# Kernel tuning notes

Measured on AMD Instinct MI355X. Metric: run time of the kernel, lower is better.

The kernel has to match this reference:

```python
import jax, jax.numpy as jnp
import numpy as np

GROUP = 32  # hadamard_group_size == MXFP4 block size
FP4_GRID = np.array([0.0, 0.5, 1.0, 1.5, 2.0, 3.0, 4.0, 6.0], dtype=np.float32)  # e2m1 magnitudes
FP4_MID = np.array([0.25, 0.75, 1.25, 1.75, 2.5, 3.5, 5.0], dtype=np.float32)    # RTN midpoints


def _hadamard(n):
    # Sylvester construction, normalized so H is orthonormal (matches hadamard(n)*n**-0.5)
    H = np.array([[1.0]], dtype=np.float64)
    while H.shape[0] < n:
        H = np.block([[H, H], [H, -H]])
    return (H / np.sqrt(n)).astype(np.float32)


def _pseudo_quant_mxfp4(t, H, gs):
    """Hadamard-rotate per group of 32, then MXFP4 (e2m1 + power-of-two block scale)
    quant-dequant with abs_max scaling and a global scale. STE through the rounding."""
    shp = t.shape
    rot = t.reshape(-1, GROUP) @ H                      # [n_groups, 32] rotated space
    v = jax.lax.stop_gradient(rot) * gs
    absmax = jnp.max(jnp.abs(v), axis=-1, keepdims=True)
    # E8M0 power-of-two shared scale so that absmax/scale <= 6 (max e2m1 value)
    scale = jnp.exp2(jnp.ceil(jnp.log2(absmax / 6.0 + 1e-30)))
    scale = jnp.where(absmax > 0, scale, 1.0)
    u = v / scale
    grid = jnp.asarray(FP4_GRID)
    mid = jnp.asarray(FP4_MID)
    q = jnp.sign(u) * grid[jnp.searchsorted(mid, jnp.abs(u))]  # round-to-nearest e2m1
    dq = q * scale / gs
    out = rot + jax.lax.stop_gradient(dq - rot)         # straight-through estimator
    return out.reshape(shp)


def setup_inputs() -> dict:
    key = jax.random.key(0)
    kx, kw, kb = jax.random.split(key, 3)
    B, S, K, N = 4, 2048, 4096, 4096
    x = jax.random.normal(kx, (B, S, K), jnp.float32)
    weight = jax.random.normal(kw, (N, K), jnp.float32) * (K ** -0.5)
    bias = jax.random.normal(kb, (N,), jnp.float32)
    H = jnp.asarray(_hadamard(GROUP))
    weight_global_scale = jnp.array([3.0], jnp.float32)  # abs_max method
    act_global_scale = jnp.array([3.0], jnp.float32)
    return {"x": x, "weight": weight, "bias": bias, "hadamard_matrix": H,
            "weight_global_scale": weight_global_scale, "act_global_scale": act_global_scale}


def reference(x, weight, bias, hadamard_matrix, weight_global_scale, act_global_scale):
    x_dq = _pseudo_quant_mxfp4(x, hadamard_matrix, act_global_scale[0])
    w_dq = _pseudo_quant_mxfp4(weight, hadamard_matrix, weight_global_scale[0])
    # both operands stay in the rotated space; per-group Hadamard is orthogonal so
    # x_rot @ w_rot^T == x @ w^T up to quantization error (QuTLASS semantics)
    return jnp.einsum('bsk,nk->bsn', x_dq, w_dq) + bias
```

## Files before the change

### kernel.cpp

```cpp
#include <hip/hip_runtime.h>
#include <hip/hip_bf16.h>

typedef int   i32x4  __attribute__((ext_vector_type(4)));
typedef int   i32x8  __attribute__((ext_vector_type(8)));
typedef float f32x16 __attribute__((ext_vector_type(16)));

__device__ inline void gload_lds16(const void* g, void* l) {
  __builtin_amdgcn_global_load_lds((const __attribute__((address_space(1))) void*)g,
                                   (__attribute__((address_space(3))) void*)l, 16, 0, 0);
}
__device__ inline void gload_lds4(const void* g, void* l) {
  __builtin_amdgcn_global_load_lds((const __attribute__((address_space(1))) void*)g,
                                   (__attribute__((address_space(3))) void*)l, 4, 0, 0);
}
__device__ inline i32x8 pad8(i32x4 v) {
  i32x8 r;
  r[0] = v[0]; r[1] = v[1]; r[2] = v[2]; r[3] = v[3];
  r[4] = 0; r[5] = 0; r[6] = 0; r[7] = 0;
  return r;
}

__global__ __launch_bounds__(256) void quant_pack_fp4(const float* __restrict__ in,
                                                      unsigned char* __restrict__ outq,
                                                      unsigned char* __restrict__ outsc,
                                                      const float* __restrict__ gs_ptr,
                                                      int n_groups, int rows, int kg) {
  int g = blockIdx.x * 256 + threadIdx.x;
  const float gs = gs_ptr[0];
  int r = g / kg, j = g - r * kg;

  float t[32];
  const float4* p4 = (const float4*)(in + (size_t)g * 32);
#pragma unroll
  for (int i = 0; i < 8; ++i) {
    float4 v4 = p4[i];
    t[4 * i + 0] = v4.x; t[4 * i + 1] = v4.y;
    t[4 * i + 2] = v4.z; t[4 * i + 3] = v4.w;
  }
#pragma unroll
  for (int s = 0; s < 5; ++s) {
    const int hh = 1 << s;
#pragma unroll
    for (int i = 0; i < 32; ++i) {
      if ((i & hh) == 0) {
        float a = t[i], b = t[i + hh];
        t[i] = a + b;
        t[i + hh] = a - b;
      }
    }
  }

  const float c = 0.17677669529663687f;
  float v[32];
  float am = 0.0f;
#pragma unroll
  for (int i = 0; i < 32; ++i) {
    float vi = (t[i] * c) * gs;
    v[i] = vi;
    am = fmaxf(am, fabsf(vi));
  }

  float a6 = am / 6.0f;
  int ex;
  float mant = frexpf(a6, &ex);
  int e = (mant == 0.5f) ? ex - 1 : ex;
  if (e < -127) e = -127;
  if (e > 127) e = 127;
  float inv_s = ldexpf(1.0f, -e);

  unsigned int dw[4] = {0u, 0u, 0u, 0u};
#pragma unroll
  for (int i = 0; i < 32; ++i) {
    float u = v[i] * inv_s;
    float au = fabsf(u);
    int idx = (au > 0.25f) + (au > 0.75f) + (au > 1.25f) + (au > 1.75f)
            + (au > 2.5f) + (au > 3.5f) + (au > 5.0f);
    int code = idx | ((u < 0.0f) ? 8 : 0);
    dw[i >> 3] |= (unsigned)code << ((i & 7) * 4);
  }
  i32x4 packed;
  packed[0] = (int)dw[0]; packed[1] = (int)dw[1];
  packed[2] = (int)dw[2]; packed[3] = (int)dw[3];
  *(i32x4*)(outq + (size_t)r * ((size_t)kg * 16) + (size_t)j * 16) = packed;

  int s = j >> 3, j0 = j & 7;
  int p = ((j0 & 1) << 2) | (j0 >> 1);
  if (kg == 128) {
    __shared__ unsigned char sl[256];
    sl[(s << 4) | ((r & 1) << 3) | p] = (unsigned char)(e + 127);
    __syncthreads();
    if (threadIdx.x < 64) {
      int si = threadIdx.x >> 2, wd = threadIdx.x & 3;
      unsigned int vv = *(const unsigned int*)&sl[(si << 4) | (wd << 2)];
      size_t r0 = (size_t)blockIdx.x * 2;
      *(unsigned int*)(outsc + ((size_t)si * rows + r0) * 8 + (wd << 2)) = vv;
    }
  } else {
    outsc[((size_t)s * rows + r) * 8 + p] = (unsigned char)(e + 127);
  }
}


#define STAGE(mb, kt, h, ldsHalf) do {                                               \
    const unsigned char* _s = (mb) + (size_t)((h)*64 + (w << 3) + (l >> 3)) * KB2    \
                      + (size_t)(kt) * 128 + (size_t)csw * 16;                       \
    gload_lds16(_s, (unsigned char*)(ldsHalf) + (w << 10));                          \
    gload_lds16(_s + ((size_t)KB2 << 5), (unsigned char*)(ldsHalf) + (w << 10) + 4096); \
  } while (0)

#define STAGE_ASC(kt, bf) gload_lds4(AscG + ((size_t)(kt) * M + brow) * 8 + (tid << 2), \
                                     (unsigned char*)&asc[bf][0] + (w << 8))
#define STAGE_BSC(kt, bf) gload_lds4(BscG + ((size_t)(kt) * N + bcol) * 8 + (tid << 2), \
                                     (unsigned char*)&bsc[bf][0] + (w << 8))

#define LOADB(bf) do {                                                               \
    const unsigned char* _bb = &lds[bf][1][0][0];                                    \
    _Pragma("unroll")                                                                \
    for (int nt = 0; nt < 2; ++nt) {                                                 \
      int row = wn * 64 + nt * 32 + (l & 31);                                        \
      int xr = row & 7;                                                              \
      _Pragma("unroll")                                                              \
      for (int kk = 0; kk < 4; ++kk)                                                 \
        bfr[nt][kk] = *(const i32x4*)(_bb + row * 128 + (((kk * 2 + h) ^ xr) << 4)); \
      sb[nt] = *(const int*)((const unsigned char*)&bsc[bf][0] + row * 8 + h * 4);   \
    } } while (0)

#define LOADA(bf, mt) do {                                                           \
    const unsigned char* _ab = &lds[bf][0][0][0];                                    \
    int row = wm * 64 + (mt) * 32 + (l & 31);                                        \
    int xr = row & 7;                                                                \
    _Pragma("unroll")                                                                \
    for (int kk = 0; kk < 4; ++kk)                                                   \
      af[kk] = *(const i32x4*)(_ab + row * 128 + (((kk * 2 + h) ^ xr) << 4));        \
    sa = *(const int*)((const unsigned char*)&asc[bf][0] + row * 8 + h * 4);         \
  } while (0)

#define MF1(mt, nt, kk)                                                              \
  acc[mt][nt] = __builtin_amdgcn_mfma_scale_f32_32x32x64_f8f6f4(                     \
      pad8(af[kk]), pad8(bfr[nt][kk]), acc[mt][nt], 4, 4, kk, sa, kk, sb[nt]);

#define MFMAQ(mt) do {                                                               \
    __builtin_amdgcn_s_setprio(1);                                                   \
    MF1(mt, 0, 0) MF1(mt, 1, 0) MF1(mt, 0, 1) MF1(mt, 1, 1)                          \
    MF1(mt, 0, 2) MF1(mt, 1, 2) MF1(mt, 0, 3) MF1(mt, 1, 3)                          \
    __builtin_amdgcn_s_setprio(0);                                                   \
  } while (0)

#define MIDSYNC() do { __builtin_amdgcn_s_barrier();                                 \
    asm volatile("s_waitcnt lgkmcnt(0)" ::: "memory");                               \
    __builtin_amdgcn_sched_barrier(0); } while (0)

#define ENDP() __builtin_amdgcn_s_barrier()
#define VM10() asm volatile("s_waitcnt vmcnt(10)" ::: "memory")

__global__ __launch_bounds__(256, 2) void gemm128_fp4(const unsigned char* __restrict__ Aq,
                                                      const unsigned char* __restrict__ Bq,
                                                      const unsigned char* __restrict__ AscG,
                                                      const unsigned char* __restrict__ BscG,
                                                      float* __restrict__ C,
                                                      const float* __restrict__ bias,
                                                      const float* __restrict__ gsx,
                                                      const float* __restrict__ gsw,
                                                      int M, int N, int K) {
  __shared__ __align__(16) unsigned char lds[2][2][2][8192];
  __shared__ __align__(16) unsigned char asc[2][1024];
  __shared__ __align__(16) unsigned char bsc[2][1024];

  const int tid = threadIdx.x;
  const int w = tid >> 6, l = tid & 63;
  const int wm = w >> 1, wn = w & 1;
  const int h = l >> 5;
  const int csw = (l & 7) ^ (l >> 3);
  const int KB2 = K >> 1;

  const int ntn = N >> 7;
  const int nwg = gridDim.x;
  int r_t, c_t;
  {
    int bid = blockIdx.x;
    if ((nwg & 7) == 0) {
      int x = bid & 7, o = bid >> 3, cpx = nwg >> 3;
      int rpx = cpx / ntn;
      if ((ntn & 7) == 0 && rpx > 0 && (cpx % ntn) == 0) {
        int g8 = o & 7, rr = (o >> 3) % rpx, ss = o / (8 * rpx);
        r_t = x * rpx + rr;
        c_t = ss * 8 + g8;
      } else {
        int lin = x * cpx + o;
        r_t = lin / ntn; c_t = lin % ntn;
      }
    } else {
      r_t = bid / ntn; c_t = bid % ntn;
    }
  }
  const size_t brow = (size_t)r_t * 128;
  const size_t bcol = (size_t)c_t * 128;

  const unsigned char* Ab = Aq + brow * (size_t)KB2;
  const unsigned char* Bb = Bq + bcol * (size_t)KB2;

  f32x16 acc[2][2];
#pragma unroll
  for (int m = 0; m < 2; ++m)
#pragma unroll
    for (int n = 0; n < 2; ++n)
#pragma unroll
      for (int r = 0; r < 16; ++r) acc[m][n][r] = 0.0f;

  i32x4 af[4], bfr[2][4];
  int sa, sb[2];

  const int nkt = K / 256;

  STAGE(Ab, 0, 0, &lds[0][0][0][0]); STAGE(Ab, 0, 1, &lds[0][0][1][0]); STAGE_ASC(0, 0);
  STAGE(Bb, 0, 0, &lds[0][1][0][0]); STAGE(Bb, 0, 1, &lds[0][1][1][0]); STAGE_BSC(0, 0);
  STAGE(Bb, 1, 0, &lds[1][1][0][0]); STAGE(Bb, 1, 1, &lds[1][1][1][0]); STAGE_BSC(1, 1);
  STAGE(Ab, 1, 0, &lds[1][0][0][0]); STAGE(Ab, 1, 1, &lds[1][0][1][0]); STAGE_ASC(1, 1);
  VM10();
  __builtin_amdgcn_s_barrier();

  for (int t = 0; t < nkt; ++t) {
    const int p = t & 1;
    const int t2 = (t + 2 < nkt) ? t + 2 : nkt - 1;

    LOADB(p); LOADA(p, 0);
    MIDSYNC();
    STAGE(Bb, t2, 0, &lds[p][1][0][0]);
    STAGE(Bb, t2, 1, &lds[p][1][1][0]);
    STAGE_BSC(t2, p);
    MFMAQ(0);
    ENDP();

    LOADA(p, 1);
    MIDSYNC();
    STAGE(Ab, t2, 0, &lds[p][0][0][0]);
    STAGE(Ab, t2, 1, &lds[p][0][1][0]);
    STAGE_ASC(t2, p);
    MFMAQ(1);
    VM10();
    ENDP();
  }

  const float inv = 1.0f / (gsx[0] * gsw[0]);
#pragma unroll
  for (int nt = 0; nt < 2; ++nt) {
    const int col = (int)bcol + wn * 64 + nt * 32 + (l & 31);
    const float bv = bias[col];
#pragma unroll
    for (int mt = 0; mt < 2; ++mt) {
      const size_t rbase = brow + (size_t)(wm * 64 + mt * 32 + 4 * h);
#pragma unroll
      for (int r = 0; r < 16; ++r) {
        const size_t row = rbase + (r & 3) + 8 * (r >> 2);
        C[row * (size_t)N + col] = acc[mt][nt][r] * inv + bv;
      }
    }
  }
}

extern "C" void kernel_launch(void* const* d_in, const int* in_sizes, int n_in,
                              void* d_out, int out_size, void* d_ws, size_t ws_size,
                              hipStream_t stream) {
  const float* x    = (const float*)d_in[0];
  const float* wgt  = (const float*)d_in[1];
  const float* bias = (const float*)d_in[2];
  const float* wgs  = (const float*)d_in[4];
  const float* ags  = (const float*)d_in[5];

  const int N = in_sizes[2];
  const int K = in_sizes[1] / N;
  const int M = in_sizes[0] / K;
  const int kg = K / 32;

  unsigned char* aq  = (unsigned char*)d_ws;
  unsigned char* bq  = aq + (size_t)M * (K / 2);
  unsigned char* asc = bq + (size_t)N * (K / 2);
  unsigned char* bsc = asc + (size_t)M * kg;

  const int xg = in_sizes[0] / 32;
  const int wg = in_sizes[1] / 32;
  quant_pack_fp4<<<dim3((xg + 255) / 256), dim3(256), 0, stream>>>(x, aq, asc, ags, xg, M, kg);
  quant_pack_fp4<<<dim3((wg + 255) / 256), dim3(256), 0, stream>>>(wgt, bq, bsc, wgs, wg, N, kg);

  dim3 grid((M / 128) * (N / 128));
  gemm128_fp4<<<grid, dim3(256), 0, stream>>>(aq, bq, asc, bsc, (float*)d_out, bias,
                                              ags, wgs, M, N, K);
}
```

Measured before the change: 155.9 us.

## Double-buffer MFMA fragments in registers and fuse the two quant kernels

The GEMM main loop now processes two K-tiles per iteration. It keeps two register sets of A/B fragments and scales, so LDS reads for the next tile are issued while MFMAs run on the current one. Each stage loads a full A+B tile set at once, with adjusted vmcnt/lgkmcnt waits and fewer barriers per tile. Separately, the activation and weight quantization kernels are merged into a single launch that picks its input by block index. This removes one launch and lets the two quantizations overlap. The cost is more register pressure from the doubled fragment storage, which may affect occupancy at two blocks per CU.

```diff
diff --git a/kernel.cpp b/kernel.cpp
--- a/kernel.cpp
+++ b/kernel.cpp
@@ -20,14 +20,25 @@
   return r;
 }
 
-__global__ __launch_bounds__(256) void quant_pack_fp4(const float* __restrict__ in,
-                                                      unsigned char* __restrict__ outq,
-                                                      unsigned char* __restrict__ outsc,
-                                                      const float* __restrict__ gs_ptr,
-                                                      int n_groups, int rows, int kg) {
-  int g = blockIdx.x * 256 + threadIdx.x;
-  const float gs = gs_ptr[0];
-  int r = g / kg, j = g - r * kg;
+__global__ __launch_bounds__(256) void quant_fused(const float* __restrict__ x,
+                                                   const float* __restrict__ wt,
+                                                   unsigned char* __restrict__ xq,
+                                                   unsigned char* __restrict__ xsc,
+                                                   unsigned char* __restrict__ wq,
+                                                   unsigned char* __restrict__ wsc,
+                                                   const float* __restrict__ ags,
+                                                   const float* __restrict__ wgs,
+                                                   int xg, int Mrows, int Nrows, int kg) {
+  const int first = blockIdx.x * 256;
+  const bool isX = first < xg;
+  const float* in        = isX ? x   : wt;
+  unsigned char* outq    = isX ? xq  : wq;
+  unsigned char* outsc   = isX ? xsc : wsc;
+  const float gs         = isX ? ags[0] : wgs[0];
+  const int rows         = isX ? Mrows : Nrows;
+  const int base         = isX ? first : first - xg;
+  const int g = base + threadIdx.x;
+  const int r = g / kg, j = g - r * kg;
 
   float t[32];
   const float4* p4 = (const float4*)(in + (size_t)g * 32);
@@ -92,7 +103,7 @@
     if (threadIdx.x < 64) {
       int si = threadIdx.x >> 2, wd = threadIdx.x & 3;
       unsigned int vv = *(const unsigned int*)&sl[(si << 4) | (wd << 2)];
-      size_t r0 = (size_t)blockIdx.x * 2;
+      size_t r0 = (size_t)(base / 128);
       *(unsigned int*)(outsc + ((size_t)si * rows + r0) * 8 + (wd << 2)) = vv;
     }
   } else {
@@ -113,7 +124,14 @@
 #define STAGE_BSC(kt, bf) gload_lds4(BscG + ((size_t)(kt) * N + bcol) * 8 + (tid << 2), \
                                      (unsigned char*)&bsc[bf][0] + (w << 8))
 
-#define LOADB(bf) do {                                                               \
+#define STAGESET(kt, bf) do {                                                        \
+    STAGE(Ab, kt, 0, &lds[bf][0][0][0]); STAGE(Ab, kt, 1, &lds[bf][0][1][0]);        \
+    STAGE_ASC(kt, bf);                                                               \
+    STAGE(Bb, kt, 0, &lds[bf][1][0][0]); STAGE(Bb, kt, 1, &lds[bf][1][1][0]);        \
+    STAGE_BSC(kt, bf);                                                               \
+  } while (0)
+
+#define READFRAGS(bf, AF, BF, SA, SB) do {                                           \
     const unsigned char* _bb = &lds[bf][1][0][0];                                    \
     _Pragma("unroll")                                                                \
     for (int nt = 0; nt < 2; ++nt) {                                                 \
@@ -121,37 +139,41 @@
       int xr = row & 7;                                                              \
       _Pragma("unroll")                                                              \
       for (int kk = 0; kk < 4; ++kk)                                                 \
-        bfr[nt][kk] = *(const i32x4*)(_bb + row * 128 + (((kk * 2 + h) ^ xr) << 4)); \
-      sb[nt] = *(const int*)((const unsigned char*)&bsc[bf][0] + row * 8 + h * 4);   \
-    } } while (0)
-
-#define LOADA(bf, mt) do {                                                           \
+        BF[nt][kk] = *(const i32x4*)(_bb + row * 128 + (((kk * 2 + h) ^ xr) << 4));  \
+      SB[nt] = *(const int*)((const unsigned char*)&bsc[bf][0] + row * 8 + h * 4);   \
+    }                                                                                \
     const unsigned char* _ab = &lds[bf][0][0][0];                                    \
-    int row = wm * 64 + (mt) * 32 + (l & 31);                                        \
-    int xr = row & 7;                                                                \
     _Pragma("unroll")                                                                \
-    for (int kk = 0; kk < 4; ++kk)                                                   \
-      af[kk] = *(const i32x4*)(_ab + row * 128 + (((kk * 2 + h) ^ xr) << 4));        \
-    sa = *(const int*)((const unsigned char*)&asc[bf][0] + row * 8 + h * 4);         \
+    for (int mt = 0; mt < 2; ++mt) {                                                 \
+      int row = wm * 64 + mt * 32 + (l & 31);                                        \
+      int xr = row & 7;                                                              \
+      _Pragma("unroll")                                                              \
+      for (int kk = 0; kk < 4; ++kk)                                                 \
+        AF[mt][kk] = *(const i32x4*)(_ab + row * 128 + (((kk * 2 + h) ^ xr) << 4));  \
+      SA[mt] = *(const int*)((const unsigned char*)&asc[bf][0] + row * 8 + h * 4);   \
+    }                                                                                \
   } while (0)
 
-#define MF1(mt, nt, kk)                                                              \
+#define MF1(AF, BF, SA, SB, mt, nt, kk)                                              \
   acc[mt][nt] = __builtin_amdgcn_mfma_scale_f32_32x32x64_f8f6f4(                     \
-      pad8(af[kk]), pad8(bfr[nt][kk]), acc[mt][nt], 4, 4, kk, sa, kk, sb[nt]);
-
-#define MFMAQ(mt) do {                                                               \
+      pad8(AF[mt][kk]), pad8(BF[nt][kk]), acc[mt][nt], 4, 4, kk, SA[mt], kk, SB[nt]);
+
+#define MFMAQ_ALL(AF, BF, SA, SB) do {                                               \
     __builtin_amdgcn_s_setprio(1);                                                   \
-    MF1(mt, 0, 0) MF1(mt, 1, 0) MF1(mt, 0, 1) MF1(mt, 1, 1)                          \
-    MF1(mt, 0, 2) MF1(mt, 1, 2) MF1(mt, 0, 3) MF1(mt, 1, 3)                          \
+    MF1(AF, BF, SA, SB, 0, 0, 0) MF1(AF, BF, SA, SB, 0, 1, 0)                        \
+    MF1(AF, BF, SA, SB, 1, 0, 0) MF1(AF, BF, SA, SB, 1, 1, 0)                        \
+    MF1(AF, BF, SA, SB, 0, 0, 1) MF1(AF, BF, SA, SB, 0, 1, 1)                        \
+    MF1(AF, BF, SA, SB, 1, 0, 1) MF1(AF, BF, SA, SB, 1, 1, 1)                        \
+    MF1(AF, BF, SA, SB, 0, 0, 2) MF1(AF, BF, SA, SB, 0, 1, 2)                        \
+    MF1(AF, BF, SA, SB, 1, 0, 2) MF1(AF, BF, SA, SB, 1, 1, 2)                        \
+    MF1(AF, BF, SA, SB, 0, 0, 3) MF1(AF, BF, SA, SB, 0, 1, 3)                        \
+    MF1(AF, BF, SA, SB, 1, 0, 3) MF1(AF, BF, SA, SB, 1, 1, 3)                        \
     __builtin_amdgcn_s_setprio(0);                                                   \
   } while (0)
 
-#define MIDSYNC() do { __builtin_amdgcn_s_barrier();                                 \
-    asm volatile("s_waitcnt lgkmcnt(0)" ::: "memory");                               \
+#define LGKM0() do { asm volatile("s_waitcnt lgkmcnt(0)" ::: "memory");              \
     __builtin_amdgcn_sched_barrier(0); } while (0)
-
-#define ENDP() __builtin_amdgcn_s_barrier()
-#define VM10() asm volatile("s_waitcnt vmcnt(10)" ::: "memory")
+#define VM6()  asm volatile("s_waitcnt vmcnt(6)" ::: "memory")
 
 __global__ __launch_bounds__(256, 2) void gemm128_fp4(const unsigned char* __restrict__ Aq,
                                                       const unsigned char* __restrict__ Bq,
@@ -207,38 +229,38 @@
 #pragma unroll
       for (int r = 0; r < 16; ++r) acc[m][n][r] = 0.0f;
 
-  i32x4 af[4], bfr[2][4];
-  int sa, sb[2];
+  i32x4 afA[2][4], bfrA[2][4];  int saA[2], sbA[2];
+  i32x4 afB[2][4], bfrB[2][4];  int saB[2], sbB[2];
 
   const int nkt = K / 256;
 
-  STAGE(Ab, 0, 0, &lds[0][0][0][0]); STAGE(Ab, 0, 1, &lds[0][0][1][0]); STAGE_ASC(0, 0);
-  STAGE(Bb, 0, 0, &lds[0][1][0][0]); STAGE(Bb, 0, 1, &lds[0][1][1][0]); STAGE_BSC(0, 0);
-  STAGE(Bb, 1, 0, &lds[1][1][0][0]); STAGE(Bb, 1, 1, &lds[1][1][1][0]); STAGE_BSC(1, 1);
-  STAGE(Ab, 1, 0, &lds[1][0][0][0]); STAGE(Ab, 1, 1, &lds[1][0][1][0]); STAGE_ASC(1, 1);
-  VM10();
+  STAGESET(0, 0);
+  STAGESET(1, 1);
+  VM6();
   __builtin_amdgcn_s_barrier();
-
-  for (int t = 0; t < nkt; ++t) {
-    const int p = t & 1;
+  READFRAGS(0, afA, bfrA, saA, sbA);
+  LGKM0();
+  __builtin_amdgcn_s_barrier();
+
+  for (int t = 0; t < nkt; t += 2) {
     const int t2 = (t + 2 < nkt) ? t + 2 : nkt - 1;
-
-    LOADB(p); LOADA(p, 0);
-    MIDSYNC();
-    STAGE(Bb, t2, 0, &lds[p][1][0][0]);
-    STAGE(Bb, t2, 1, &lds[p][1][1][0]);
-    STAGE_BSC(t2, p);
-    MFMAQ(0);
-    ENDP();
-
-    LOADA(p, 1);
-    MIDSYNC();
-    STAGE(Ab, t2, 0, &lds[p][0][0][0]);
-    STAGE(Ab, t2, 1, &lds[p][0][1][0]);
-    STAGE_ASC(t2, p);
-    MFMAQ(1);
-    VM10();
-    ENDP();
+    const int t3 = (t + 3 < nkt) ? t + 3 : nkt - 1;
+
+    STAGESET(t2, 0);
+    VM6();
+    __builtin_amdgcn_s_barrier();
+    READFRAGS(1, afB, bfrB, saB, sbB);
+    MFMAQ_ALL(afA, bfrA, saA, sbA);
+    LGKM0();
+    __builtin_amdgcn_s_barrier();
+
+    STAGESET(t3, 1);
+    VM6();
+    __builtin_amdgcn_s_barrier();
+    READFRAGS(0, afA, bfrA, saA, sbA);
+    MFMAQ_ALL(afB, bfrB, saB, sbB);
+    LGKM0();
+    __builtin_amdgcn_s_barrier();
   }
 
   const float inv = 1.0f / (gsx[0] * gsw[0]);
@@ -279,8 +301,8 @@
 
   const int xg = in_sizes[0] / 32;
   const int wg = in_sizes[1] / 32;
-  quant_pack_fp4<<<dim3((xg + 255) / 256), dim3(256), 0, stream>>>(x, aq, asc, ags, xg, M, kg);
-  quant_pack_fp4<<<dim3((wg + 255) / 256), dim3(256), 0, stream>>>(wgt, bq, bsc, wgs, wg, N, kg);
+  quant_fused<<<dim3((xg + wg) / 256), dim3(256), 0, stream>>>(
+      x, wgt, aq, asc, bq, bsc, ags, wgs, xg, M, N, kg);
 
   dim3 grid((M / 128) * (N / 128));
   gemm128_fp4<<<grid, dim3(256), 0, stream>>>(aq, bq, asc, bsc, (float*)d_out, bias,
```

New measurement: 166.0 us. 6.5% more time.

## Load B operand directly from global to registers and fuse quant launches

Applied to the files above, without the earlier changes.

The GEMM no longer stages the B tile and its scales through LDS. Each wave reads its B fragments and scales straight from global memory into two register sets, which double-buffer B across k-tiles. The main loop is unrolled by two and the vmcnt wait threshold is raised to match the extra loads. The two quantization launches are merged into one grid that splits blocks between x and the weight, removing a kernel launch. In exchange, B is read uncoalesced from global memory and replicated across waves, and register pressure rises.

```diff
diff --git a/kernel.cpp b/kernel.cpp
--- a/kernel.cpp
+++ b/kernel.cpp
@@ -20,14 +20,25 @@
   return r;
 }
 
-__global__ __launch_bounds__(256) void quant_pack_fp4(const float* __restrict__ in,
-                                                      unsigned char* __restrict__ outq,
-                                                      unsigned char* __restrict__ outsc,
-                                                      const float* __restrict__ gs_ptr,
-                                                      int n_groups, int rows, int kg) {
-  int g = blockIdx.x * 256 + threadIdx.x;
-  const float gs = gs_ptr[0];
-  int r = g / kg, j = g - r * kg;
+__global__ __launch_bounds__(256) void quant_fused(const float* __restrict__ x,
+                                                   const float* __restrict__ wt,
+                                                   unsigned char* __restrict__ xq,
+                                                   unsigned char* __restrict__ xsc,
+                                                   unsigned char* __restrict__ wq,
+                                                   unsigned char* __restrict__ wsc,
+                                                   const float* __restrict__ ags,
+                                                   const float* __restrict__ wgs,
+                                                   int xg, int Mrows, int Nrows, int kg) {
+  const int first = blockIdx.x * 256;
+  const bool isX = first < xg;
+  const float* in        = isX ? x   : wt;
+  unsigned char* outq    = isX ? xq  : wq;
+  unsigned char* outsc   = isX ? xsc : wsc;
+  const float gs         = isX ? ags[0] : wgs[0];
+  const int rows         = isX ? Mrows : Nrows;
+  const int base         = isX ? first : first - xg;
+  const int g = base + threadIdx.x;
+  const int r = g / kg, j = g - r * kg;
 
   float t[32];
   const float4* p4 = (const float4*)(in + (size_t)g * 32);
@@ -92,7 +103,7 @@
     if (threadIdx.x < 64) {
       int si = threadIdx.x >> 2, wd = threadIdx.x & 3;
       unsigned int vv = *(const unsigned int*)&sl[(si << 4) | (wd << 2)];
-      size_t r0 = (size_t)blockIdx.x * 2;
+      size_t r0 = (size_t)(base / 128);
       *(unsigned int*)(outsc + ((size_t)si * rows + r0) * 8 + (wd << 2)) = vv;
     }
   } else {
@@ -101,8 +112,8 @@
 }
 
 
-#define STAGE(mb, kt, h, ldsHalf) do {                                               \
-    const unsigned char* _s = (mb) + (size_t)((h)*64 + (w << 3) + (l >> 3)) * KB2    \
+#define STAGE_A(kt, h, ldsHalf) do {                                                 \
+    const unsigned char* _s = Ab + (size_t)((h)*64 + (w << 3) + (l >> 3)) * KB2      \
                       + (size_t)(kt) * 128 + (size_t)csw * 16;                       \
     gload_lds16(_s, (unsigned char*)(ldsHalf) + (w << 10));                          \
     gload_lds16(_s + ((size_t)KB2 << 5), (unsigned char*)(ldsHalf) + (w << 10) + 4096); \
@@ -110,23 +121,25 @@
 
 #define STAGE_ASC(kt, bf) gload_lds4(AscG + ((size_t)(kt) * M + brow) * 8 + (tid << 2), \
                                      (unsigned char*)&asc[bf][0] + (w << 8))
-#define STAGE_BSC(kt, bf) gload_lds4(BscG + ((size_t)(kt) * N + bcol) * 8 + (tid << 2), \
-                                     (unsigned char*)&bsc[bf][0] + (w << 8))
-
-#define LOADB(bf) do {                                                               \
-    const unsigned char* _bb = &lds[bf][1][0][0];                                    \
+
+#define STAGESET_A(kt, bf) do {                                                      \
+    STAGE_A(kt, 0, &lds[bf][0][0]); STAGE_A(kt, 1, &lds[bf][1][0]);                  \
+    STAGE_ASC(kt, bf);                                                               \
+  } while (0)
+
+#define LOADBF(kt, BF, SB) do {                                                      \
     _Pragma("unroll")                                                                \
     for (int nt = 0; nt < 2; ++nt) {                                                 \
       int row = wn * 64 + nt * 32 + (l & 31);                                        \
-      int xr = row & 7;                                                              \
+      const unsigned char* _bp = Bb + (size_t)row * KB2 + (size_t)(kt) * 128 + (h << 4); \
       _Pragma("unroll")                                                              \
       for (int kk = 0; kk < 4; ++kk)                                                 \
-        bfr[nt][kk] = *(const i32x4*)(_bb + row * 128 + (((kk * 2 + h) ^ xr) << 4)); \
-      sb[nt] = *(const int*)((const unsigned char*)&bsc[bf][0] + row * 8 + h * 4);   \
+        BF[nt][kk] = *(const i32x4*)(_bp + (kk << 5));                               \
+      SB[nt] = *(const int*)(BscG + ((size_t)(kt) * N + bcol + row) * 8 + (h << 2)); \
     } } while (0)
 
 #define LOADA(bf, mt) do {                                                           \
-    const unsigned char* _ab = &lds[bf][0][0][0];                                    \
+    const unsigned char* _ab = &lds[bf][0][0];                                       \
     int row = wm * 64 + (mt) * 32 + (l & 31);                                        \
     int xr = row & 7;                                                                \
     _Pragma("unroll")                                                                \
@@ -135,14 +148,16 @@
     sa = *(const int*)((const unsigned char*)&asc[bf][0] + row * 8 + h * 4);         \
   } while (0)
 
-#define MF1(mt, nt, kk)                                                              \
+#define MF1(mt, nt, kk, BF, SB)                                                      \
   acc[mt][nt] = __builtin_amdgcn_mfma_scale_f32_32x32x64_f8f6f4(                     \
-      pad8(af[kk]), pad8(bfr[nt][kk]), acc[mt][nt], 4, 4, kk, sa, kk, sb[nt]);
-
-#define MFMAQ(mt) do {                                                               \
+      pad8(af[kk]), pad8(BF[nt][kk]), acc[mt][nt], 4, 4, kk, sa, kk, SB[nt]);
+
+#define MFMAQ(mt, BF, SB) do {                                                       \
     __builtin_amdgcn_s_setprio(1);                                                   \
-    MF1(mt, 0, 0) MF1(mt, 1, 0) MF1(mt, 0, 1) MF1(mt, 1, 1)                          \
-    MF1(mt, 0, 2) MF1(mt, 1, 2) MF1(mt, 0, 3) MF1(mt, 1, 3)                          \
+    MF1(mt, 0, 0, BF, SB) MF1(mt, 1, 0, BF, SB)                                      \
+    MF1(mt, 0, 1, BF, SB) MF1(mt, 1, 1, BF, SB)                                      \
+    MF1(mt, 0, 2, BF, SB) MF1(mt, 1, 2, BF, SB)                                      \
+    MF1(mt, 0, 3, BF, SB) MF1(mt, 1, 3, BF, SB)                                      \
     __builtin_amdgcn_s_setprio(0);                                                   \
   } while (0)
 
@@ -151,7 +166,7 @@
     __builtin_amdgcn_sched_barrier(0); } while (0)
 
 #define ENDP() __builtin_amdgcn_s_barrier()
-#define VM10() asm volatile("s_waitcnt vmcnt(10)" ::: "memory")
+#define VM13() asm volatile("s_waitcnt vmcnt(13)" ::: "memory")
 
 __global__ __launch_bounds__(256, 2) void gemm128_fp4(const unsigned char* __restrict__ Aq,
                                                       const unsigned char* __restrict__ Bq,
@@ -162,9 +177,8 @@
                                                       const float* __restrict__ gsx,
                                                       const float* __restrict__ gsw,
                                                       int M, int N, int K) {
-  __shared__ __align__(16) unsigned char lds[2][2][2][8192];
+  __shared__ __align__(16) unsigned char lds[2][2][8192];
   __shared__ __align__(16) unsigned char asc[2][1024];
-  __shared__ __align__(16) unsigned char bsc[2][1024];
 
   const int tid = threadIdx.x;
   const int w = tid >> 6, l = tid & 63;
@@ -207,37 +221,41 @@
 #pragma unroll
       for (int r = 0; r < 16; ++r) acc[m][n][r] = 0.0f;
 
-  i32x4 af[4], bfr[2][4];
-  int sa, sb[2];
+  i32x4 af[4];
+  int sa;
+  i32x4 bfX[2][4], bfY[2][4];
+  int sbX[2], sbY[2];
 
   const int nkt = K / 256;
 
-  STAGE(Ab, 0, 0, &lds[0][0][0][0]); STAGE(Ab, 0, 1, &lds[0][0][1][0]); STAGE_ASC(0, 0);
-  STAGE(Bb, 0, 0, &lds[0][1][0][0]); STAGE(Bb, 0, 1, &lds[0][1][1][0]); STAGE_BSC(0, 0);
-  STAGE(Bb, 1, 0, &lds[1][1][0][0]); STAGE(Bb, 1, 1, &lds[1][1][1][0]); STAGE_BSC(1, 1);
-  STAGE(Ab, 1, 0, &lds[1][0][0][0]); STAGE(Ab, 1, 1, &lds[1][0][1][0]); STAGE_ASC(1, 1);
-  VM10();
+  STAGESET_A(0, 0);
+  STAGESET_A(1, 1);
+  LOADBF(0, bfX, sbX);
+  VM13();
   __builtin_amdgcn_s_barrier();
 
-  for (int t = 0; t < nkt; ++t) {
-    const int p = t & 1;
+  for (int i = 0; i < nkt / 2; ++i) {
+    const int t = 2 * i;
+    const int t1 = t + 1;
     const int t2 = (t + 2 < nkt) ? t + 2 : nkt - 1;
-
-    LOADB(p); LOADA(p, 0);
+    const int t3 = (t + 3 < nkt) ? t + 3 : nkt - 1;
+
+    LOADA(0, 0); LOADBF(t1, bfY, sbY);
+    MIDSYNC(); MFMAQ(0, bfX, sbX); ENDP();
+    LOADA(0, 1);
     MIDSYNC();
-    STAGE(Bb, t2, 0, &lds[p][1][0][0]);
-    STAGE(Bb, t2, 1, &lds[p][1][1][0]);
-    STAGE_BSC(t2, p);
-    MFMAQ(0);
+    STAGESET_A(t2, 0);
+    MFMAQ(1, bfX, sbX);
+    VM13();
     ENDP();
 
-    LOADA(p, 1);
+    LOADA(1, 0); LOADBF(t2, bfX, sbX);
+    MIDSYNC(); MFMAQ(0, bfY, sbY); ENDP();
+    LOADA(1, 1);
     MIDSYNC();
-    STAGE(Ab, t2, 0, &lds[p][0][0][0]);
-    STAGE(Ab, t2, 1, &lds[p][0][1][0]);
-    STAGE_ASC(t2, p);
-    MFMAQ(1);
-    VM10();
+    STAGESET_A(t3, 1);
+    MFMAQ(1, bfY, sbY);
+    VM13();
     ENDP();
   }
 
@@ -279,8 +297,8 @@
 
   const int xg = in_sizes[0] / 32;
   const int wg = in_sizes[1] / 32;
-  quant_pack_fp4<<<dim3((xg + 255) / 256), dim3(256), 0, stream>>>(x, aq, asc, ags, xg, M, kg);
-  quant_pack_fp4<<<dim3((wg + 255) / 256), dim3(256), 0, stream>>>(wgt, bq, bsc, wgs, wg, N, kg);
+  quant_fused<<<dim3((xg + wg) / 256), dim3(256), 0, stream>>>(
+      x, wgt, aq, asc, bq, bsc, ags, wgs, xg, M, N, kg);
 
   dim3 grid((M / 128) * (N / 128));
   gemm128_fp4<<<grid, dim3(256), 0, stream>>>(aq, bq, asc, bsc, (float*)d_out, bias,
```

After: 214.1 us. 1.37x slower.
